# Kernel tuning notes

Measured on AMD Instinct MI355X. Metric: run time of the kernel, lower is better.

The kernel has to match this reference:

```python
import jax, jax.numpy as jnp
import numpy as np

N_NODES = 100000
N_EDGES = 1600000
IN_FEAT = 64
OUT_FEAT = 64
NUM_RELS = 8
NUM_BASES = 4


def setup_inputs() -> dict:
    key = jax.random.key(0)
    ks = jax.random.split(key, 9)
    feat = jax.random.normal(ks[0], (N_NODES, IN_FEAT), dtype=jnp.float32)
    src = jax.random.randint(ks[1], (N_EDGES,), 0, N_NODES, dtype=jnp.int64)
    dst = jax.random.randint(ks[2], (N_EDGES,), 0, N_NODES, dtype=jnp.int64)
    etypes = jax.random.randint(ks[3], (N_EDGES,), 0, NUM_RELS, dtype=jnp.int64)
    norm = jax.random.uniform(ks[4], (N_EDGES, 1), dtype=jnp.float32)
    # learned parameters (xavier-uniform-like scaling)
    def xavier(k, shape):
        fan_in, fan_out = shape[-2], shape[-1]
        lim = jnp.sqrt(6.0 / (fan_in + fan_out)).astype(jnp.float32)
        return jax.random.uniform(k, shape, jnp.float32, -lim, lim)
    weight = xavier(ks[5], (NUM_BASES, IN_FEAT, OUT_FEAT))
    w_comp = xavier(ks[6], (NUM_RELS, NUM_BASES))
    h_bias = jnp.zeros((OUT_FEAT,), dtype=jnp.float32)
    loop_weight = xavier(ks[7], (IN_FEAT, OUT_FEAT))
    return {"feat": feat, "src": src, "dst": dst, "etypes": etypes,
            "norm": norm, "weight": weight, "w_comp": w_comp,
            "h_bias": h_bias, "loop_weight": loop_weight}


def reference(feat, src, dst, etypes, norm, weight, w_comp, h_bias, loop_weight):
    # Basis decomposition: W_r = sum_b w_comp[r,b] * V_b.
    # Per-edge message m_e = feat[src_e] @ W_{etype_e} * norm_e, computed as:
    #   proj[n,b,:] = feat[n] @ V_b   (project nodes once per basis)
    #   m_e = sum_b w_comp[etype_e, b] * proj[src_e, b, :]
    # which is mathematically identical and avoids an [E, in, out] weight gather.
    proj = jnp.einsum('ni,bio->nbo', feat, weight)      # [N, B, out]
    coef = w_comp[etypes]                               # [E, B]
    msg = jnp.einsum('eb,ebo->eo', coef, proj[src])     # [E, out]
    msg = msg * norm                                    # edge normalizer
    # Aggregate (sum) into destination nodes
    agg = jax.ops.segment_sum(msg, dst, num_segments=feat.shape[0])  # [N, out]
    # bias + self-loop message
    out = agg + h_bias + feat @ loop_weight
    return out
```

## Files before the change

### kernel.cpp

```cpp
#include <hip/hip_runtime.h>
#include <hip/hip_bf16.h>


constexpr int NNODES = 100000;
constexpr int NEDGES = 1600000;

constexpr size_t WF_BYTES  = (size_t)NNODES * 512 * 2;
constexpr size_t HEADE_OFF = WF_BYTES;
constexpr size_t REC_OFF   = HEADE_OFF + (size_t)NNODES * 4;
constexpr size_t WS_NEED_E = REC_OFF + (size_t)NEDGES * 16;
constexpr size_t WCAT_OFF  = WS_NEED_E;
constexpr size_t WS_NEED_M = WCAT_OFF + (size_t)576 * 64 * 2;
constexpr size_t HEAD_OFF  = WF_BYTES;
constexpr size_t NEXT_OFF  = HEAD_OFF + (size_t)NNODES * 4;
constexpr size_t WS_NEED   = NEXT_OFF + (size_t)NEDGES * 4;

typedef __attribute__((ext_vector_type(8))) short short8v;
typedef __attribute__((ext_vector_type(4))) float f32x4;

__global__ __launch_bounds__(256)
void k_wcat(const float* __restrict__ weight, const float* __restrict__ w_comp,
            const float* __restrict__ loop_w, __hip_bfloat16* __restrict__ wcat)
{
    const int idx = blockIdx.x * 256 + threadIdx.x;
    if (idx >= 576 * 64) return;
    const int c = idx >> 6, i = idx & 63;
    float v;
    if (c < 512) {
        const int r = c >> 6, o = c & 63;
        v = w_comp[r * 4 + 0] * weight[        i * 64 + o]
          + w_comp[r * 4 + 1] * weight[ 4096 + i * 64 + o]
          + w_comp[r * 4 + 2] * weight[ 8192 + i * 64 + o]
          + w_comp[r * 4 + 3] * weight[12288 + i * 64 + o];
    } else {
        v = loop_w[i * 64 + (c - 512)];
    }
    wcat[(size_t)c * 64 + i] = __float2bfloat16(v);
}

__global__ __launch_bounds__(256)
void proj_mfma(const float* __restrict__ feat,
               const __hip_bfloat16* __restrict__ wcat,
               const float* __restrict__ h_bias,
               __hip_bfloat16* __restrict__ wfeat,
               float* __restrict__ out)
{
    __shared__ __hip_bfloat16 Alds[32 * 72];
    __shared__ __hip_bfloat16 Clds[32 * 520];

    const int t = threadIdx.x;
    const int lane = t & 63;
    const int wv = t >> 6;
    const int nbase = blockIdx.x * 32;

    {
        const float4* fsrc = (const float4*)(feat + (size_t)nbase * 64);
        #pragma unroll
        for (int kk = 0; kk < 2; ++kk) {
            const int idx = t + kk * 256;
            const float4 f = fsrc[idx];
            const int row = idx >> 4;
            const int c4  = (idx & 15) * 4;
            __hip_bfloat16* p = &Alds[row * 72 + c4];
            p[0] = __float2bfloat16(f.x);
            p[1] = __float2bfloat16(f.y);
            p[2] = __float2bfloat16(f.z);
            p[3] = __float2bfloat16(f.w);
        }
    }
    __syncthreads();

    const int colbase = wv * 144;
    const int lr = lane & 15;
    const int lg = lane >> 4;

    f32x4 acc[2][9];
    #pragma unroll
    for (int mf = 0; mf < 2; ++mf)
        #pragma unroll
        for (int nf = 0; nf < 9; ++nf)
            acc[mf][nf] = (f32x4){0.f, 0.f, 0.f, 0.f};

    #pragma unroll
    for (int ks = 0; ks < 2; ++ks) {
        short8v a[2];
        #pragma unroll
        for (int mf = 0; mf < 2; ++mf)
            a[mf] = *(const short8v*)&Alds[(mf * 16 + lr) * 72 + ks * 32 + lg * 8];
        short8v b[9];
        #pragma unroll
        for (int nf = 0; nf < 9; ++nf) {
            const int col = colbase + nf * 16 + lr;
            b[nf] = *(const short8v*)&wcat[(size_t)col * 64 + ks * 32 + lg * 8];
        }
        #pragma unroll
        for (int mf = 0; mf < 2; ++mf)
            #pragma unroll
            for (int nf = 0; nf < 9; ++nf)
                acc[mf][nf] = __builtin_amdgcn_mfma_f32_16x16x32_bf16(
                    a[mf], b[nf], acc[mf][nf], 0, 0, 0);
    }

    #pragma unroll
    for (int mf = 0; mf < 2; ++mf) {
        #pragma unroll
        for (int nf = 0; nf < 9; ++nf) {
            const int gc = colbase + nf * 16 + lr;
            const int mrow = mf * 16 + lg * 4;
            if (gc < 512) {
                #pragma unroll
                for (int q = 0; q < 4; ++q)
                    Clds[(mrow + q) * 520 + gc] = __float2bfloat16(acc[mf][nf][q]);
            } else {
                const int o = gc - 512;
                const float bias = h_bias[o];
                #pragma unroll
                for (int q = 0; q < 4; ++q)
                    out[(size_t)(nbase + mrow + q) * 64 + o] = bias + acc[mf][nf][q];
            }
        }
    }
    __syncthreads();

    #pragma unroll
    for (int p = 0; p < 8; ++p) {
        const int node = p * 4 + wv;
        const uint4 v = *(const uint4*)&Clds[node * 520 + lane * 8];
        *(uint4*)((char*)(wfeat + (size_t)(nbase + node) * 512) + lane * 16) = v;
    }
}

__global__ __launch_bounds__(256)
void k_link_emb(const int* __restrict__ src, const int* __restrict__ dst,
                const int* __restrict__ et, const float* __restrict__ norm,
                int* __restrict__ head, int4* __restrict__ rec)
{
    const int i = blockIdx.x * blockDim.x + threadIdx.x;
    const int stride = gridDim.x * blockDim.x;
    for (int e = i; e < NEDGES; e += stride) {
        const int d = dst[e];
        const int s = src[e];
        const int r = et[e];
        const float nm = norm[e];
        const int old = atomicExch(&head[d], e);
        rec[e] = make_int4(old, s * 512 + r * 64, __float_as_int(nm), 0);
    }
}

__global__ __launch_bounds__(256)
void k_agg_emb(const int* __restrict__ head, const int4* __restrict__ rec,
               const __hip_bfloat16* __restrict__ wfeat,
               float* __restrict__ out)
{
    const int lane = threadIdx.x & 63;
    const int wid = (int)((blockIdx.x * blockDim.x + threadIdx.x) >> 6);
    const int n0 = wid * 8;

    int   e[8];
    float acc[8];
    bool alive = false;
    #pragma unroll
    for (int k = 0; k < 8; ++k) {
        e[k] = head[n0 + k];
        acc[k] = 0.0f;
        alive = alive || (e[k] >= 0);
    }

    while (alive) {
        int4 R[8];
        #pragma unroll
        for (int k = 0; k < 8; ++k) {
            const int idx = (e[k] >= 0) ? e[k] : 0;
            R[k] = rec[idx];
        }
        float w[8];
        #pragma unroll
        for (int k = 0; k < 8; ++k)
            w[k] = __bfloat162float(wfeat[(size_t)R[k].y + lane]);
        alive = false;
        #pragma unroll
        for (int k = 0; k < 8; ++k) {
            if (e[k] >= 0) {
                acc[k] = fmaf(__int_as_float(R[k].z), w[k], acc[k]);
                e[k] = R[k].x;
            }
            alive = alive || (e[k] >= 0);
        }
    }

    #pragma unroll
    for (int k = 0; k < 8; ++k)
        out[(size_t)(n0 + k) * 64 + lane] += acc[k];
}

template <int PATH>
__global__ __launch_bounds__(256)
void rgcn_proj(const float* __restrict__ feat,
               const float* __restrict__ weight,
               const float* __restrict__ w_comp,
               const float* __restrict__ h_bias,
               const float* __restrict__ loop_w,
               __hip_bfloat16* __restrict__ table,
               float* __restrict__ out)
{
    __shared__ float featl[32 * 64];

    const int t = threadIdx.x;
    const int nbase = blockIdx.x * 32;

    {
        const float4* fsrc = (const float4*)(feat + (size_t)nbase * 64);
        float4* fdst = (float4*)featl;
        fdst[t] = fsrc[t];
        fdst[t + 256] = fsrc[t + 256];
    }

    const int lane = t & 63;
    const int n0 = (t >> 6) * 8;
    const float bias = h_bias[lane];

    __syncthreads();

    constexpr int NM = (PATH == 2) ? 1 : 5;
    float acc[8][NM];
    #pragma unroll
    for (int n = 0; n < 8; ++n)
        #pragma unroll
        for (int m = 0; m < NM; ++m)
            acc[n][m] = 0.0f;

    #pragma unroll 4
    for (int i0 = 0; i0 < 64; i0 += 4) {
        float4 f4[8];
        #pragma unroll
        for (int n = 0; n < 8; ++n)
            f4[n] = *(const float4*)&featl[(n0 + n) * 64 + i0];
        #pragma unroll
        for (int q = 0; q < 4; ++q) {
            const int i = i0 + q;
            float vv[NM];
            if (PATH < 2) {
                #pragma unroll
                for (int b = 0; b < 4; ++b)
                    vv[b] = weight[b * 4096 + i * 64 + lane];
                vv[4] = loop_w[i * 64 + lane];
            } else {
                vv[0] = loop_w[i * 64 + lane];
            }
            #pragma unroll
            for (int n = 0; n < 8; ++n) {
                const float fv = (q == 0) ? f4[n].x : (q == 1) ? f4[n].y
                               : (q == 2) ? f4[n].z : f4[n].w;
                #pragma unroll
                for (int m = 0; m < NM; ++m)
                    acc[n][m] = fmaf(fv, vv[m], acc[n][m]);
            }
        }
    }

    float wc[8][4];
    if (PATH == 0) {
        #pragma unroll
        for (int r = 0; r < 8; ++r)
            #pragma unroll
            for (int b = 0; b < 4; ++b)
                wc[r][b] = w_comp[r * 4 + b];
    }

    #pragma unroll
    for (int n = 0; n < 8; ++n) {
        const size_t gn = (size_t)(nbase + n0 + n);
        out[gn * 64 + lane] = bias + acc[n][NM - 1];
        if (PATH == 0) {
            #pragma unroll
            for (int r = 0; r < 8; ++r) {
                const float w = fmaf(wc[r][0], acc[n][0],
                                fmaf(wc[r][1], acc[n][1],
                                fmaf(wc[r][2], acc[n][2],
                                     wc[r][3] * acc[n][3])));
                table[gn * 512 + (size_t)r * 64 + lane] = __float2bfloat16(w);
            }
        } else if (PATH == 1) {
            #pragma unroll
            for (int b = 0; b < 4; ++b)
                table[gn * 256 + (size_t)b * 64 + lane] = __float2bfloat16(acc[n][b]);
        }
    }
}

__global__ __launch_bounds__(256)
void k_link(const int* __restrict__ dst, int* __restrict__ head,
            int* __restrict__ next)
{
    const int i = blockIdx.x * blockDim.x + threadIdx.x;
    const int stride = gridDim.x * blockDim.x;
    for (int e = i; e < NEDGES; e += stride) {
        const int d = dst[e];
        const int old = atomicExch(&head[d], e);
        next[e] = old;
    }
}

__global__ __launch_bounds__(256)
void k_agg(const int* __restrict__ head, const int* __restrict__ next,
           const int* __restrict__ src, const int* __restrict__ et,
           const float* __restrict__ norm,
           const __hip_bfloat16* __restrict__ wfeat,
           float* __restrict__ out)
{
    const int lane = threadIdx.x & 63;
    const int wid = (int)((blockIdx.x * blockDim.x + threadIdx.x) >> 6);
    const int n0 = wid * 8;

    int   e[8];
    float acc[8];
    #pragma unroll
    for (int k = 0; k < 8; ++k) {
        e[k] = head[n0 + k];
        acc[k] = 0.0f;
    }

    while (true) {
        bool progress = false;
        #pragma unroll
        for (int k = 0; k < 8; ++k) {
            const int ek = e[k];
            if (ek >= 0) {
                progress = true;
                const int   s = src[ek];
                const int   r = et[ek];
                const float m = norm[ek];
                const float w = __bfloat162float(
                    wfeat[(size_t)s * 512 + (size_t)r * 64 + lane]);
                acc[k] = fmaf(m, w, acc[k]);
                e[k] = next[ek];
            }
        }
        if (!progress) break;
    }

    #pragma unroll
    for (int k = 0; k < 8; ++k)
        out[(size_t)(n0 + k) * 64 + lane] += acc[k];
}

__global__ __launch_bounds__(256)
void rgcn_edge_a(const int* __restrict__ src, const int* __restrict__ dst,
                 const int* __restrict__ et, const float* __restrict__ norm,
                 const __hip_bfloat16* __restrict__ wfeat,
                 float* __restrict__ out)
{
    const int lane = threadIdx.x & 63;
    const int wid  = (int)((blockIdx.x * blockDim.x + threadIdx.x) >> 6);
    const int nw   = (int)((gridDim.x * blockDim.x) >> 6);
    for (int e = wid; e < NEDGES; e += nw) {
        const int   s  = src[e];
        const int   d  = dst[e];
        const int   r  = et[e];
        const float nm = norm[e];
        const float w  = __bfloat162float(wfeat[(size_t)s * 512 + (size_t)r * 64 + lane]);
        atomicAdd(out + (size_t)d * 64 + lane, w * nm);
    }
}

__global__ __launch_bounds__(256)
void rgcn_edge_b(const int* __restrict__ src, const int* __restrict__ dst,
                 const int* __restrict__ et, const float* __restrict__ norm,
                 const __hip_bfloat16* __restrict__ proj,
                 const float* __restrict__ w_comp,
                 float* __restrict__ out)
{
    const int lane = threadIdx.x & 63;
    const int wid  = (int)((blockIdx.x * blockDim.x + threadIdx.x) >> 6);
    const int nw   = (int)((gridDim.x * blockDim.x) >> 6);
    for (int e = wid; e < NEDGES; e += nw) {
        const int   s  = src[e];
        const int   d  = dst[e];
        const int   r  = et[e];
        const float nm = norm[e];
        const __hip_bfloat16* p = proj + (size_t)s * 256;
        float m = w_comp[r * 4 + 0] * __bfloat162float(p[lane]);
        m = fmaf(w_comp[r * 4 + 1], __bfloat162float(p[ 64 + lane]), m);
        m = fmaf(w_comp[r * 4 + 2], __bfloat162float(p[128 + lane]), m);
        m = fmaf(w_comp[r * 4 + 3], __bfloat162float(p[192 + lane]), m);
        atomicAdd(out + (size_t)d * 64 + lane, m * nm);
    }
}

__global__ __launch_bounds__(256)
void rgcn_edge_c(const int* __restrict__ src, const int* __restrict__ dst,
                 const int* __restrict__ et, const float* __restrict__ norm,
                 const float* __restrict__ feat,
                 const float* __restrict__ weight,
                 const float* __restrict__ w_comp,
                 float* __restrict__ out)
{
    __shared__ __hip_bfloat16 Vl[4 * 64 * 64];
    const int t = threadIdx.x;
    #pragma unroll
    for (int k = 0; k < 64; ++k)
        Vl[t + k * 256] = __float2bfloat16(weight[t + k * 256]);
    __syncthreads();

    const int lane = t & 63;
    const int wid  = (int)((blockIdx.x * blockDim.x + t) >> 6);
    const int nw   = (int)((gridDim.x * blockDim.x) >> 6);
    for (int e = wid; e < NEDGES; e += nw) {
        const int   s  = src[e];
        const int   d  = dst[e];
        const int   r  = et[e];
        const float nm = norm[e];
        const float wc0 = w_comp[r * 4 + 0], wc1 = w_comp[r * 4 + 1];
        const float wc2 = w_comp[r * 4 + 2], wc3 = w_comp[r * 4 + 3];
        const float f = feat[(size_t)s * 64 + lane];
        float acc = 0.0f;
        #pragma unroll 8
        for (int i = 0; i < 64; ++i) {
            const float fi = __shfl(f, i);
            float w =        wc0 * __bfloat162float(Vl[          i * 64 + lane]);
            w = fmaf(wc1, __bfloat162float(Vl[ 4096 + i * 64 + lane]), w);
            w = fmaf(wc2, __bfloat162float(Vl[ 8192 + i * 64 + lane]), w);
            w = fmaf(wc3, __bfloat162float(Vl[12288 + i * 64 + lane]), w);
            acc = fmaf(fi, w, acc);
        }
        atomicAdd(out + (size_t)d * 64 + lane, acc * nm);
    }
}

extern "C" void kernel_launch(void* const* d_in, const int* in_sizes, int n_in,
                              void* d_out, int out_size, void* d_ws, size_t ws_size,
                              hipStream_t stream) {
    const float* feat   = (const float*)d_in[0];
    const int*   src    = (const int*)  d_in[1];
    const int*   dst    = (const int*)  d_in[2];
    const int*   et     = (const int*)  d_in[3];
    const float* norm   = (const float*)d_in[4];
    const float* weight = (const float*)d_in[5];
    const float* w_comp = (const float*)d_in[6];
    const float* h_bias = (const float*)d_in[7];
    const float* loop_w = (const float*)d_in[8];
    float* out = (float*)d_out;
    char* ws = (char*)d_ws;

    const dim3 gridP(NNODES / 32);

    if (ws_size >= WS_NEED_M) {
        __hip_bfloat16* wfeat = (__hip_bfloat16*)ws;
        int*  head = (int*)(ws + HEADE_OFF);
        int4* rec  = (int4*)(ws + REC_OFF);
        __hip_bfloat16* wcat = (__hip_bfloat16*)(ws + WCAT_OFF);

        hipMemsetAsync(head, 0xFF, (size_t)NNODES * 4, stream);
        hipLaunchKernelGGL(k_wcat, dim3(144), dim3(256), 0, stream,
                           weight, w_comp, loop_w, wcat);
        hipLaunchKernelGGL(k_link_emb, dim3(2048), dim3(256), 0, stream,
                           src, dst, et, norm, head, rec);
        hipLaunchKernelGGL(proj_mfma, gridP, dim3(256), 0, stream,
                           feat, wcat, h_bias, wfeat, out);
        hipLaunchKernelGGL(k_agg_emb, dim3(NNODES / 32), dim3(256), 0, stream,
                           head, rec, wfeat, out);
    } else if (ws_size >= WS_NEED_E) {
        __hip_bfloat16* wfeat = (__hip_bfloat16*)ws;
        int*  head = (int*)(ws + HEADE_OFF);
        int4* rec  = (int4*)(ws + REC_OFF);

        hipMemsetAsync(head, 0xFF, (size_t)NNODES * 4, stream);
        hipLaunchKernelGGL(k_link_emb, dim3(2048), dim3(256), 0, stream,
                           src, dst, et, norm, head, rec);
        hipLaunchKernelGGL((rgcn_proj<0>), gridP, dim3(256), 0, stream,
                           feat, weight, w_comp, h_bias, loop_w, wfeat, out);
        hipLaunchKernelGGL(k_agg_emb, dim3(NNODES / 32), dim3(256), 0, stream,
                           head, rec, wfeat, out);
    } else if (ws_size >= WS_NEED) {
        __hip_bfloat16* wfeat = (__hip_bfloat16*)ws;
        int* head = (int*)(ws + HEAD_OFF);
        int* next = (int*)(ws + NEXT_OFF);

        hipMemsetAsync(head, 0xFF, (size_t)NNODES * 4, stream);
        hipLaunchKernelGGL(k_link, dim3(2048), dim3(256), 0, stream,
                           dst, head, next);
        hipLaunchKernelGGL((rgcn_proj<0>), gridP, dim3(256), 0, stream,
                           feat, weight, w_comp, h_bias, loop_w, wfeat, out);
        hipLaunchKernelGGL(k_agg, dim3(NNODES / 32), dim3(256), 0, stream,
                           head, next, src, et, norm, wfeat, out);
    } else if (ws_size >= WF_BYTES) {
        __hip_bfloat16* wfeat = (__hip_bfloat16*)ws;
        hipLaunchKernelGGL((rgcn_proj<0>), gridP, dim3(256), 0, stream,
                           feat, weight, w_comp, h_bias, loop_w, wfeat, out);
        hipLaunchKernelGGL(rgcn_edge_a, dim3(2048), dim3(256), 0, stream,
                           src, dst, et, norm, wfeat, out);
    } else if (ws_size >= (size_t)NNODES * 256 * 2) {
        __hip_bfloat16* proj = (__hip_bfloat16*)ws;
        hipLaunchKernelGGL((rgcn_proj<1>), gridP, dim3(256), 0, stream,
                           feat, weight, w_comp, h_bias, loop_w, proj, out);
        hipLaunchKernelGGL(rgcn_edge_b, dim3(2048), dim3(256), 0, stream,
                           src, dst, et, norm, proj, w_comp, out);
    } else {
        hipLaunchKernelGGL((rgcn_proj<2>), gridP, dim3(256), 0, stream,
                           feat, weight, w_comp, h_bias, loop_w,
                           (__hip_bfloat16*)nullptr, out);
        hipLaunchKernelGGL(rgcn_edge_c, dim3(2048), dim3(256), 0, stream,
                           src, dst, et, norm, feat, weight, w_comp, out);
    }
}
```

Before: 316.8 us.

## Fuse edge-linking and MFMA projection into one role-split kernel launch

Merges the edge linked-list build (atomicExch on head plus record write) and the MFMA node projection into a single kernel. Every third block runs the linking loop and the other two run the projection tile, so memory- and atomic-latency-bound work can overlap with compute-bound work and one launch goes away. The cost is that the linking blocks still reserve the projection's large LDS allocation, which can lower occupancy. The linking now uses fewer threads (1562 blocks instead of 2048), so each thread handles more edges.

```diff
diff --git a/kernel.cpp b/kernel.cpp
--- a/kernel.cpp
+++ b/kernel.cpp
@@ -39,19 +39,41 @@
 }
 
 __global__ __launch_bounds__(256)
-void proj_mfma(const float* __restrict__ feat,
-               const __hip_bfloat16* __restrict__ wcat,
-               const float* __restrict__ h_bias,
-               __hip_bfloat16* __restrict__ wfeat,
-               float* __restrict__ out)
+void k_fused(const float* __restrict__ feat,
+             const __hip_bfloat16* __restrict__ wcat,
+             const float* __restrict__ h_bias,
+             __hip_bfloat16* __restrict__ wfeat,
+             float* __restrict__ out,
+             const int* __restrict__ src, const int* __restrict__ dst,
+             const int* __restrict__ et, const float* __restrict__ norm,
+             int* __restrict__ head, int4* __restrict__ rec)
 {
     __shared__ __hip_bfloat16 Alds[32 * 72];
     __shared__ __hip_bfloat16 Clds[32 * 520];
 
+    const int bid = blockIdx.x;
     const int t = threadIdx.x;
+    const int g = bid / 3;
+    const int rrole = bid - g * 3;
+
+    if (rrole == 2) {
+        const int i = g * 256 + t;
+        const int stride = 1562 * 256;
+        for (int e = i; e < NEDGES; e += stride) {
+            const int d = dst[e];
+            const int s = src[e];
+            const int rr = et[e];
+            const float nm = norm[e];
+            const int old = atomicExch(&head[d], e);
+            rec[e] = make_int4(old, s * 512 + rr * 64, __float_as_int(nm), 0);
+        }
+        return;
+    }
+
+    const int pidx = g * 2 + rrole;
     const int lane = t & 63;
     const int wv = t >> 6;
-    const int nbase = blockIdx.x * 32;
+    const int nbase = pidx * 32;
 
     {
         const float4* fsrc = (const float4*)(feat + (size_t)nbase * 64);
@@ -131,6 +153,52 @@
 }
 
 __global__ __launch_bounds__(256)
+void k_agg_emb(const int* __restrict__ head, const int4* __restrict__ rec,
+               const __hip_bfloat16* __restrict__ wfeat,
+               float* __restrict__ out)
+{
+    const int lane = threadIdx.x & 63;
+    const int wid = (int)((blockIdx.x * blockDim.x + threadIdx.x) >> 6);
+    const int n0 = wid * 8;
+
+    int   e[8];
+    float acc[8];
+    bool alive = false;
+    #pragma unroll
+    for (int k = 0; k < 8; ++k) {
+        e[k] = head[n0 + k];
+        acc[k] = 0.0f;
+        alive = alive || (e[k] >= 0);
+    }
+
+    while (alive) {
+        int4 R[8];
+        #pragma unroll
+        for (int k = 0; k < 8; ++k) {
+            const int idx = (e[k] >= 0) ? e[k] : 0;
+            R[k] = rec[idx];
+        }
+        float w[8];
+        #pragma unroll
+        for (int k = 0; k < 8; ++k)
+            w[k] = __bfloat162float(wfeat[(size_t)R[k].y + lane]);
+        alive = false;
+        #pragma unroll
+        for (int k = 0; k < 8; ++k) {
+            if (e[k] >= 0) {
+                acc[k] = fmaf(__int_as_float(R[k].z), w[k], acc[k]);
+                e[k] = R[k].x;
+            }
+            alive = alive || (e[k] >= 0);
+        }
+    }
+
+    #pragma unroll
+    for (int k = 0; k < 8; ++k)
+        out[(size_t)(n0 + k) * 64 + lane] += acc[k];
+}
+
+__global__ __launch_bounds__(256)
 void k_link_emb(const int* __restrict__ src, const int* __restrict__ dst,
                 const int* __restrict__ et, const float* __restrict__ norm,
                 int* __restrict__ head, int4* __restrict__ rec)
@@ -145,52 +213,6 @@
         const int old = atomicExch(&head[d], e);
         rec[e] = make_int4(old, s * 512 + r * 64, __float_as_int(nm), 0);
     }
-}
-
-__global__ __launch_bounds__(256)
-void k_agg_emb(const int* __restrict__ head, const int4* __restrict__ rec,
-               const __hip_bfloat16* __restrict__ wfeat,
-               float* __restrict__ out)
-{
-    const int lane = threadIdx.x & 63;
-    const int wid = (int)((blockIdx.x * blockDim.x + threadIdx.x) >> 6);
-    const int n0 = wid * 8;
-
-    int   e[8];
-    float acc[8];
-    bool alive = false;
-    #pragma unroll
-    for (int k = 0; k < 8; ++k) {
-        e[k] = head[n0 + k];
-        acc[k] = 0.0f;
-        alive = alive || (e[k] >= 0);
-    }
-
-    while (alive) {
-        int4 R[8];
-        #pragma unroll
-        for (int k = 0; k < 8; ++k) {
-            const int idx = (e[k] >= 0) ? e[k] : 0;
-            R[k] = rec[idx];
-        }
-        float w[8];
-        #pragma unroll
-        for (int k = 0; k < 8; ++k)
-            w[k] = __bfloat162float(wfeat[(size_t)R[k].y + lane]);
-        alive = false;
-        #pragma unroll
-        for (int k = 0; k < 8; ++k) {
-            if (e[k] >= 0) {
-                acc[k] = fmaf(__int_as_float(R[k].z), w[k], acc[k]);
-                e[k] = R[k].x;
-            }
-            alive = alive || (e[k] >= 0);
-        }
-    }
-
-    #pragma unroll
-    for (int k = 0; k < 8; ++k)
-        out[(size_t)(n0 + k) * 64 + lane] += acc[k];
 }
 
 template <int PATH>
@@ -453,10 +475,9 @@
         hipMemsetAsync(head, 0xFF, (size_t)NNODES * 4, stream);
         hipLaunchKernelGGL(k_wcat, dim3(144), dim3(256), 0, stream,
                            weight, w_comp, loop_w, wcat);
-        hipLaunchKernelGGL(k_link_emb, dim3(2048), dim3(256), 0, stream,
+        hipLaunchKernelGGL(k_fused, dim3(4687), dim3(256), 0, stream,
+                           feat, wcat, h_bias, wfeat, out,
                            src, dst, et, norm, head, rec);
-        hipLaunchKernelGGL(proj_mfma, gridP, dim3(256), 0, stream,
-                           feat, wcat, h_bias, wfeat, out);
         hipLaunchKernelGGL(k_agg_emb, dim3(NNODES / 32), dim3(256), 0, stream,
                            head, rec, wfeat, out);
     } else if (ws_size >= WS_NEED_E) {
```

Measured after the change: 289.4 us. -8.7%, faster.
